# Optimization experiments

Measured on AMD Instinct MI355X. Metric: run time of the kernel, lower is better.

Reference implementation:

```python
import jax, jax.numpy as jnp
import numpy as np

N, E, F_NODE, F_EDGE, H, L, G = 4096, 12288, 64, 16, 128, 4, 256
BN_EPS = 1e-5


def setup_inputs() -> dict:
    key = jax.random.key(0)
    ks = jax.random.split(key, 20)
    s = lambda k, shape, fan: jax.random.normal(k, shape, jnp.float32) * (1.0 / np.sqrt(fan))
    inp = {
        'x': jax.random.normal(ks[0], (N, F_NODE), jnp.float32),
        'edge_index': jax.random.randint(ks[1], (2, E), 0, N, dtype=jnp.int64),
        'edge_attr': jax.random.normal(ks[2], (E, F_EDGE), jnp.float32),
        'batch': jnp.sort(jax.random.randint(ks[3], (N,), 0, G, dtype=jnp.int64)),
        # node encoder
        'node_w': s(ks[4], (F_NODE, H), F_NODE),
        'node_b': jnp.zeros((H,), jnp.float32),
        # per-layer edge MLP: edge_feat -> 128 -> H*H
        'e1_w': s(ks[5], (L, F_EDGE, 128), F_EDGE),
        'e1_b': jnp.zeros((L, 128), jnp.float32),
        'e2_w': s(ks[6], (L, 128, H * H), 128) * 0.1,
        'e2_b': jnp.zeros((L, H * H), jnp.float32),
        # NNConv root weight + bias
        'root_w': s(ks[7], (L, H, H), H),
        'conv_b': jnp.zeros((L, H), jnp.float32),
        # batchnorm affine
        'bn_g': jnp.ones((L, H), jnp.float32),
        'bn_b': jnp.zeros((L, H), jnp.float32),
        # head
        'head_w1': s(ks[8], (H, H), H),
        'head_b1': jnp.zeros((H,), jnp.float32),
        'head_w2': s(ks[9], (H, 1), H),
        'head_b2': jnp.zeros((1,), jnp.float32),
    }
    return inp


def reference(x, edge_index, edge_attr, batch, node_w, node_b, e1_w, e1_b,
              e2_w, e2_b, root_w, conv_b, bn_g, bn_b, head_w1, head_b1,
              head_w2, head_b2):
    src, dst = edge_index[0], edge_index[1]
    h = x @ node_w + node_b  # [N,H]
    # in-degree for mean aggregation
    deg = jax.ops.segment_sum(jnp.ones((E,), h.dtype), dst, num_segments=N)
    inv_deg = jnp.where(deg > 0, 1.0 / jnp.maximum(deg, 1.0), 0.0)[:, None]
    for l in range(L):
        # edge MLP -> per-edge [H,H] weight
        e = jax.nn.relu(edge_attr @ e1_w[l] + e1_b[l])            # [E,128]
        W_e = (e @ e2_w[l] + e2_b[l]).reshape(E, H, H)            # [E,H,H]
        msg = jnp.einsum('eh,eho->eo', h[src], W_e)               # [E,H]
        agg = jax.ops.segment_sum(msg, dst, num_segments=N) * inv_deg
        out = agg + h @ root_w[l] + conv_b[l]
        # batchnorm (training-mode batch stats, biased var as in torch)
        mu = out.mean(0)
        var = out.var(0)
        out = (out - mu) * jax.lax.rsqrt(var + BN_EPS) * bn_g[l] + bn_b[l]
        h = h + jax.nn.relu(out)  # dropout disabled (eval)
    # global mean pool over graphs
    cnt = jax.ops.segment_sum(jnp.ones((N,), h.dtype), batch, num_segments=G)
    pooled = jax.ops.segment_sum(h, batch, num_segments=G) / jnp.maximum(cnt, 1.0)[:, None]
    y = jax.nn.relu(pooled @ head_w1 + head_b1) @ head_w2 + head_b2
    return y.squeeze(-1)  # [G]
```

## Files before the change

### kernel.cpp

```cpp
#include <hip/hip_runtime.h>

#define N_NODES 4096
#define E_TOT   12288
#define F_NODE  64
#define F_EDGE  16
#define HDIM    128
#define NLAYER  4
#define NGRAPH  256

typedef _Float16 half8 __attribute__((ext_vector_type(8)));
typedef float    f32x4 __attribute__((ext_vector_type(4)));

__global__ void k_prep_w2(const float* __restrict__ e2w, const float* __restrict__ e2b,
                          _Float16* __restrict__ W2F)
{
    int t = blockIdx.x * 256 + threadIdx.x;
    const int PER_L = 129 * 16384;
    if (t >= NLAYER * PER_L) return;
    int l   = t / PER_L;
    int r   = t - l * PER_L;
    int k   = r >> 14;
    int rem = r & 16383;
    int chunk = rem >> 9;
    int lane  = (rem >> 3) & 63;
    int j     = rem & 7;
    int hc = chunk >> 3, ot = chunk & 7;
    int h  = hc * 32 + (lane >> 4) * 8 + j;
    int o  = ot * 16 + (lane & 15);
    float v;
    if (k < 128) v = e2w[((size_t)(l * 128 + k)) * 16384 + h * 128 + o];
    else         v = e2b[(size_t)l * 16384 + h * 128 + o];
    W2F[t] = (_Float16)v;
}

__global__ __launch_bounds__(128)
void k_node_enc(const float* __restrict__ x, const float* __restrict__ nw,
                const float* __restrict__ nb, float* __restrict__ h,
                _Float16* __restrict__ hf)
{
    __shared__ float xl[F_NODE];
    int n = blockIdx.x, o = threadIdx.x;
    if (o < F_NODE) xl[o] = x[(size_t)n * F_NODE + o];
    __syncthreads();
    float acc = nb[o];
#pragma unroll 8
    for (int f = 0; f < F_NODE; ++f) acc += xl[f] * nw[f * HDIM + o];
    h [(size_t)n * HDIM + o] = acc;
    hf[(size_t)n * HDIM + o] = (_Float16)acc;
}

__global__ void k_deg(const int* __restrict__ dst, int* __restrict__ deg)
{
    int e = blockIdx.x * 256 + threadIdx.x;
    if (e < E_TOT) atomicAdd(&deg[dst[e]], 1);
}

__global__ void k_invd(const int* __restrict__ deg, float* __restrict__ invd)
{
    int n = blockIdx.x * 256 + threadIdx.x;
    if (n < N_NODES) invd[n] = deg[n] > 0 ? 1.0f / (float)deg[n] : 0.0f;
}

#define EF_STRIDE 136
__global__ __launch_bounds__(128)
void k_edge_mlp(const float* __restrict__ ea, const float* __restrict__ w1,
                const float* __restrict__ b1, _Float16* __restrict__ efg)
{
    __shared__ float al[F_EDGE];
    int e = blockIdx.x, j = threadIdx.x;
    if (j < F_EDGE) al[j] = ea[(size_t)e * F_EDGE + j];
    __syncthreads();
    float acc = b1[j];
#pragma unroll
    for (int f = 0; f < F_EDGE; ++f) acc += al[f] * w1[f * HDIM + j];
    acc = fmaxf(acc, 0.f);
    efg[(size_t)e * EF_STRIDE + j] = (_Float16)acc;
    if (j == 0) efg[(size_t)e * EF_STRIDE + 128] = (_Float16)1.0f;
}

#define BM 96
__global__ __launch_bounds__(512, 4)
void k_msg(const _Float16* __restrict__ W2L,
           const _Float16* __restrict__ efg,
           const _Float16* __restrict__ hf,
           const int* __restrict__ srcIdx,
           const int* __restrict__ dstIdx,
           float* __restrict__ agg4)
{
    __shared__ _Float16 Bb[2][16384];
    __shared__ _Float16 efs[BM][40];

    const int tid  = threadIdx.x;
    const int lane = tid & 63;
    const int w    = tid >> 6;
    const int rq   = w >> 2;
    const int ch   = w & 3;
    const int lhi  = lane >> 4;
    const int llo  = lane & 15;

    const int bx    = blockIdx.x;
    const int ks    = (bx >> 1) & 3;
    const int tile  = (bx & 1) + (bx >> 3) * 2;
    const int e0    = tile * BM;
    const int kbase = (129 * ks) >> 2;
    const int kcnt  = ((129 * (ks + 1)) >> 2) - kbase;
    float* agg = agg4 + (size_t)ks * N_NODES * HDIM;

    if (tid < BM * 5) {
        int r = tid / 5, c = tid - r * 5;
        *(half8*)&efs[r][c * 8] =
            *(const half8*)(efg + (size_t)(e0 + r) * EF_STRIDE + kbase + c * 8);
    }

    half8 hs[3][4];
#pragma unroll
    for (int rf = 0; rf < 3; ++rf) {
        int s = srcIdx[e0 + rq * 48 + rf * 16 + llo];
        const _Float16* hp = hf + (size_t)s * HDIM + lhi * 8;
#pragma unroll
        for (int hc = 0; hc < 4; ++hc)
            hs[rf][hc] = *(const half8*)(hp + hc * 32);
    }

    asm volatile("s_waitcnt vmcnt(0) lgkmcnt(0)" ::: "memory");

    auto STAGE = [&](int kg, int buf) {
        const _Float16* g = W2L + (size_t)kg * 16384 + w * 2048 + lane * 8;
        _Float16* lp = &Bb[buf][w * 2048];
#pragma unroll
        for (int i = 0; i < 4; ++i)
            __builtin_amdgcn_global_load_lds(
                (const __attribute__((address_space(1))) void*)(g + i * 512),
                (__attribute__((address_space(3))) void*)(lp + i * 512), 16, 0, 0);
    };

    STAGE(kbase + 0, 0);

    f32x4 acc[3][2];
#pragma unroll
    for (int rf = 0; rf < 3; ++rf)
#pragma unroll
        for (int cf = 0; cf < 2; ++cf)
#pragma unroll
            for (int d = 0; d < 4; ++d) acc[rf][cf][d] = 0.f;

    for (int kk = 0; kk < kcnt; ++kk) {
        const int cur = kk & 1;
        asm volatile("" ::: "memory");
        __builtin_amdgcn_s_barrier();
        asm volatile("" ::: "memory");
        if (kk + 1 < kcnt) {
            STAGE(kbase + kk + 1, cur ^ 1);
            asm volatile("s_waitcnt vmcnt(4)" ::: "memory");
        } else {
            asm volatile("s_waitcnt vmcnt(0)" ::: "memory");
        }
        asm volatile("" ::: "memory");
        __builtin_amdgcn_s_barrier();
        asm volatile("" ::: "memory");

        _Float16 efv[3];
#pragma unroll
        for (int rf = 0; rf < 3; ++rf) efv[rf] = efs[rq * 48 + rf * 16 + llo][kk];

        const _Float16* bb = &Bb[cur][ch * 1024 + lane * 8];
        __builtin_amdgcn_s_setprio(1);
#pragma unroll
        for (int hc = 0; hc < 4; ++hc) {
            half8 bfr[2];
#pragma unroll
            for (int cf = 0; cf < 2; ++cf)
                bfr[cf] = *(const half8*)(bb + hc * 4096 + cf * 512);
#pragma unroll
            for (int rf = 0; rf < 3; ++rf) {
                half8 av = hs[rf][hc] * efv[rf];
#pragma unroll
                for (int cf = 0; cf < 2; ++cf)
                    acc[rf][cf] = __builtin_amdgcn_mfma_f32_16x16x32_f16(
                        av, bfr[cf], acc[rf][cf], 0, 0, 0);
            }
        }
        __builtin_amdgcn_s_setprio(0);
    }

#pragma unroll
    for (int rf = 0; rf < 3; ++rf) {
#pragma unroll
        for (int r = 0; r < 4; ++r) {
            int row = rq * 48 + rf * 16 + lhi * 4 + r;
            int d   = dstIdx[e0 + row];
#pragma unroll
            for (int cf = 0; cf < 2; ++cf) {
                int o = ch * 32 + cf * 16 + llo;
                atomicAdd(&agg[(size_t)d * HDIM + o], acc[rf][cf][r]);
            }
        }
    }
}

__global__ __launch_bounds__(128)
void k_out(const float* __restrict__ agg4, const float* __restrict__ invd,
           const float* __restrict__ h, const float* __restrict__ rw,
           const float* __restrict__ cb, float* __restrict__ outb)
{
    __shared__ float hl[16][HDIM];
    int n0 = blockIdx.x * 16, o = threadIdx.x;
    for (int r = 0; r < 16; ++r) hl[r][o] = h[(size_t)(n0 + r) * HDIM + o];
    __syncthreads();
    float acc[16];
    float cbv = cb[o];
#pragma unroll
    for (int r = 0; r < 16; ++r) {
        float s = 0.f;
#pragma unroll
        for (int p = 0; p < 4; ++p)
            s += agg4[(size_t)p * N_NODES * HDIM + (size_t)(n0 + r) * HDIM + o];
        acc[r] = s * invd[n0 + r] + cbv;
    }
    for (int hh = 0; hh < HDIM; ++hh) {
        float wv = rw[hh * HDIM + o];
#pragma unroll
        for (int r = 0; r < 16; ++r) acc[r] += hl[r][hh] * wv;
    }
#pragma unroll
    for (int r = 0; r < 16; ++r) outb[(size_t)(n0 + r) * HDIM + o] = acc[r];
}

__global__ __launch_bounds__(256)
void k_bn_stats(const float* __restrict__ outb, float* __restrict__ mu,
                float* __restrict__ rsig)
{
    __shared__ float s1[256], s2[256];
    int c = blockIdx.x, t = threadIdx.x;
    float a = 0.f, b = 0.f;
    for (int n = t; n < N_NODES; n += 256) {
        float v = outb[(size_t)n * HDIM + c];
        a += v; b += v * v;
    }
    s1[t] = a; s2[t] = b;
    __syncthreads();
    for (int s = 128; s > 0; s >>= 1) {
        if (t < s) { s1[t] += s1[t + s]; s2[t] += s2[t + s]; }
        __syncthreads();
    }
    if (t == 0) {
        float m   = s1[0] / (float)N_NODES;
        float var = s2[0] / (float)N_NODES - m * m;
        mu[c]   = m;
        rsig[c] = rsqrtf(var + 1e-5f);
    }
}

__global__ void k_bn_apply(const float* __restrict__ outb, const float* __restrict__ mu,
                           const float* __restrict__ rsig, const float* __restrict__ g,
                           const float* __restrict__ b, float* __restrict__ h,
                           _Float16* __restrict__ hf)
{
    int i = blockIdx.x * 256 + threadIdx.x;
    int o = i & (HDIM - 1);
    float v  = (outb[i] - mu[o]) * rsig[o] * g[o] + b[o];
    float hn = h[i] + fmaxf(v, 0.f);
    h[i]  = hn;
    hf[i] = (_Float16)hn;
}

__global__ __launch_bounds__(128)
void k_pool(const float* __restrict__ h, const int* __restrict__ batch,
            float* __restrict__ pooled, int* __restrict__ cnt)
{
    int n = blockIdx.x, c = threadIdx.x;
    int g = batch[n];
    atomicAdd(&pooled[(size_t)g * HDIM + c], h[(size_t)n * HDIM + c]);
    if (c == 0) atomicAdd(&cnt[g], 1);
}

__global__ __launch_bounds__(128)
void k_head(const float* __restrict__ pooled, const int* __restrict__ cnt,
            const float* __restrict__ w1, const float* __restrict__ b1,
            const float* __restrict__ w2, const float* __restrict__ b2,
            float* __restrict__ y)
{
    __shared__ float pl[HDIM];
    __shared__ float red[HDIM];
    int g = blockIdx.x, o = threadIdx.x;
    float ic = 1.0f / (float)max(cnt[g], 1);
    pl[o] = pooled[(size_t)g * HDIM + o] * ic;
    __syncthreads();
    float t = b1[o];
#pragma unroll 8
    for (int hh = 0; hh < HDIM; ++hh) t += pl[hh] * w1[hh * HDIM + o];
    t = fmaxf(t, 0.f);
    red[o] = t * w2[o];
    __syncthreads();
    for (int s = 64; s > 0; s >>= 1) {
        if (o < s) red[o] += red[o + s];
        __syncthreads();
    }
    if (o == 0) y[g] = red[0] + b2[0];
}

extern "C" void kernel_launch(void* const* d_in, const int* in_sizes, int n_in,
                              void* d_out, int out_size, void* d_ws, size_t ws_size,
                              hipStream_t stream)
{
    const float* x      = (const float*)d_in[0];
    const int*   ei     = (const int*)  d_in[1];
    const float* ea     = (const float*)d_in[2];
    const int*   batch  = (const int*)  d_in[3];
    const float* node_w = (const float*)d_in[4];
    const float* node_b = (const float*)d_in[5];
    const float* e1w    = (const float*)d_in[6];
    const float* e1b    = (const float*)d_in[7];
    const float* e2w    = (const float*)d_in[8];
    const float* e2b    = (const float*)d_in[9];
    const float* rw     = (const float*)d_in[10];
    const float* cb     = (const float*)d_in[11];
    const float* bng    = (const float*)d_in[12];
    const float* bnb    = (const float*)d_in[13];
    const float* hw1    = (const float*)d_in[14];
    const float* hb1    = (const float*)d_in[15];
    const float* hw2    = (const float*)d_in[16];
    const float* hb2    = (const float*)d_in[17];
    float* y = (float*)d_out;

    char* ws = (char*)d_ws;
    _Float16* W2F  = (_Float16*)ws; ws += 16908288;
    float*    h    = (float*)ws;    ws += 2097152;
    _Float16* hf   = (_Float16*)ws; ws += 1048576;
    _Float16* efg  = (_Float16*)ws; ws += 3342336;
    float*    agg4 = (float*)ws;    ws += 8388608;
    float*    outb = (float*)ws;    ws += 2097152;
    int*      deg  = (int*)ws;      ws += 16384;
    float*    invd = (float*)ws;    ws += 16384;
    float*    mu   = (float*)ws;    ws += 512;
    float*    rsig = (float*)ws;    ws += 512;
    float*    pooled = (float*)ws;  ws += 131072;
    int*      cnt  = (int*)ws;      ws += 1024;

    const int* src = ei;
    const int* dst = ei + E_TOT;

    k_prep_w2<<<33024, 256, 0, stream>>>(e2w, e2b, W2F);
    k_node_enc<<<N_NODES, 128, 0, stream>>>(x, node_w, node_b, h, hf);
    hipMemsetAsync(deg, 0, N_NODES * sizeof(int), stream);
    k_deg<<<(E_TOT + 255) / 256, 256, 0, stream>>>(dst, deg);
    k_invd<<<(N_NODES + 255) / 256, 256, 0, stream>>>(deg, invd);

    for (int l = 0; l < NLAYER; ++l) {
        k_edge_mlp<<<E_TOT, 128, 0, stream>>>(ea, e1w + l * F_EDGE * HDIM,
                                              e1b + l * HDIM, efg);
        hipMemsetAsync(agg4, 0, (size_t)4 * N_NODES * HDIM * sizeof(float), stream);
        k_msg<<<(E_TOT / BM) * 4, 512, 0, stream>>>(W2F + (size_t)l * 129 * 16384,
                                                    efg, hf, src, dst, agg4);
        k_out<<<N_NODES / 16, 128, 0, stream>>>(agg4, invd, h,
                                                rw + l * HDIM * HDIM,
                                                cb + l * HDIM, outb);
        k_bn_stats<<<HDIM, 256, 0, stream>>>(outb, mu, rsig);
        k_bn_apply<<<(N_NODES * HDIM) / 256, 256, 0, stream>>>(
            outb, mu, rsig, bng + l * HDIM, bnb + l * HDIM, h, hf);
    }

    hipMemsetAsync(pooled, 0, (size_t)NGRAPH * HDIM * sizeof(float), stream);
    hipMemsetAsync(cnt, 0, NGRAPH * sizeof(int), stream);
    k_pool<<<N_NODES, 128, 0, stream>>>(h, batch, pooled, cnt);
    k_head<<<NGRAPH, 128, 0, stream>>>(pooled, cnt, hw1, hb1, hw2, hb2, y);
}
```

Measured before the change: 471.3 us.

## Load W2 directly into registers in k_msg, batch edge MLP, fuse BN stats

The message kernel drops the LDS double-buffer of W2 and has each wave load its own B fragments from global memory into registers, prefetching the next k-slice while issuing MFMAs. Tiles shrink to 64 edges with 256 threads, and each wave now covers all rows for a 32-column slice. The edge MLP processes 16 edges per block with weights cached in LDS and writes vectorized half8 outputs. BatchNorm statistics are accumulated with atomics inside k_out, which removes the separate stats kernel; the buffers are zeroed by extending the agg4 memset. The trade-offs are more global/L2 traffic for W2, since it is no longer shared across waves through LDS, and less precise one-pass variance.

```diff
diff --git a/kernel.cpp b/kernel.cpp
--- a/kernel.cpp
+++ b/kernel.cpp
@@ -62,24 +62,37 @@
 }
 
 #define EF_STRIDE 136
-__global__ __launch_bounds__(128)
+__global__ __launch_bounds__(256)
 void k_edge_mlp(const float* __restrict__ ea, const float* __restrict__ w1,
                 const float* __restrict__ b1, _Float16* __restrict__ efg)
 {
-    __shared__ float al[F_EDGE];
-    int e = blockIdx.x, j = threadIdx.x;
-    if (j < F_EDGE) al[j] = ea[(size_t)e * F_EDGE + j];
-    __syncthreads();
-    float acc = b1[j];
-#pragma unroll
-    for (int f = 0; f < F_EDGE; ++f) acc += al[f] * w1[f * HDIM + j];
-    acc = fmaxf(acc, 0.f);
-    efg[(size_t)e * EF_STRIDE + j] = (_Float16)acc;
-    if (j == 0) efg[(size_t)e * EF_STRIDE + 128] = (_Float16)1.0f;
-}
-
-#define BM 96
-__global__ __launch_bounds__(512, 4)
+    __shared__ float al[16][17];
+    __shared__ float wl[16][HDIM];
+    __shared__ float bl[HDIM];
+    int t = threadIdx.x, e0 = blockIdx.x * 16;
+    if (t < HDIM) bl[t] = b1[t];
+    for (int i = t; i < F_EDGE * HDIM; i += 256) wl[i >> 7][i & 127] = w1[i];
+    { int i = t; al[i >> 4][i & 15] = ea[(size_t)e0 * F_EDGE + i]; }
+    __syncthreads();
+    int e = t >> 4, og = t & 15;
+    float acc[8];
+#pragma unroll
+    for (int j = 0; j < 8; ++j) acc[j] = bl[og * 8 + j];
+#pragma unroll
+    for (int f = 0; f < F_EDGE; ++f) {
+        float a = al[e][f];
+#pragma unroll
+        for (int j = 0; j < 8; ++j) acc[j] += a * wl[f][og * 8 + j];
+    }
+    half8 o;
+#pragma unroll
+    for (int j = 0; j < 8; ++j) o[j] = (_Float16)fmaxf(acc[j], 0.f);
+    *(half8*)&efg[(size_t)(e0 + e) * EF_STRIDE + og * 8] = o;
+    if (og == 0) efg[(size_t)(e0 + e) * EF_STRIDE + 128] = (_Float16)1.0f;
+}
+
+#define BM 64
+__global__ __launch_bounds__(256, 3)
 void k_msg(const _Float16* __restrict__ W2L,
            const _Float16* __restrict__ efg,
            const _Float16* __restrict__ hf,
@@ -87,111 +100,100 @@
            const int* __restrict__ dstIdx,
            float* __restrict__ agg4)
 {
-    __shared__ _Float16 Bb[2][16384];
     __shared__ _Float16 efs[BM][40];
 
     const int tid  = threadIdx.x;
     const int lane = tid & 63;
     const int w    = tid >> 6;
-    const int rq   = w >> 2;
-    const int ch   = w & 3;
     const int lhi  = lane >> 4;
     const int llo  = lane & 15;
 
     const int bx    = blockIdx.x;
-    const int ks    = (bx >> 1) & 3;
-    const int tile  = (bx & 1) + (bx >> 3) * 2;
+    const int ks    = (bx & 7) >> 1;
+    const int tile  = (bx >> 3) * 2 + (bx & 1);
     const int e0    = tile * BM;
     const int kbase = (129 * ks) >> 2;
     const int kcnt  = ((129 * (ks + 1)) >> 2) - kbase;
     float* agg = agg4 + (size_t)ks * N_NODES * HDIM;
 
-    if (tid < BM * 5) {
-        int r = tid / 5, c = tid - r * 5;
+    for (int i = tid; i < BM * 5; i += 256) {
+        int r = i / 5, c = i - r * 5;
         *(half8*)&efs[r][c * 8] =
             *(const half8*)(efg + (size_t)(e0 + r) * EF_STRIDE + kbase + c * 8);
     }
 
-    half8 hs[3][4];
-#pragma unroll
-    for (int rf = 0; rf < 3; ++rf) {
-        int s = srcIdx[e0 + rq * 48 + rf * 16 + llo];
+    half8 hs[4][4];
+#pragma unroll
+    for (int rf = 0; rf < 4; ++rf) {
+        int s = srcIdx[e0 + rf * 16 + llo];
         const _Float16* hp = hf + (size_t)s * HDIM + lhi * 8;
 #pragma unroll
         for (int hc = 0; hc < 4; ++hc)
             hs[rf][hc] = *(const half8*)(hp + hc * 32);
     }
 
-    asm volatile("s_waitcnt vmcnt(0) lgkmcnt(0)" ::: "memory");
-
-    auto STAGE = [&](int kg, int buf) {
-        const _Float16* g = W2L + (size_t)kg * 16384 + w * 2048 + lane * 8;
-        _Float16* lp = &Bb[buf][w * 2048];
-#pragma unroll
-        for (int i = 0; i < 4; ++i)
-            __builtin_amdgcn_global_load_lds(
-                (const __attribute__((address_space(1))) void*)(g + i * 512),
-                (__attribute__((address_space(3))) void*)(lp + i * 512), 16, 0, 0);
-    };
-
-    STAGE(kbase + 0, 0);
-
-    f32x4 acc[3][2];
-#pragma unroll
-    for (int rf = 0; rf < 3; ++rf)
+    __syncthreads();
+
+    const _Float16* bp = W2L + (size_t)kbase * 16384 + (w * 2) * 512 + lane * 8;
+
+#define LDH(dst, kk, h2) do {                                          \
+        const _Float16* p_ = bp + (size_t)(kk) * 16384 + (h2) * 8192;  \
+        dst[0] = *(const half8*)(p_);                                  \
+        dst[1] = *(const half8*)(p_ + 512);                            \
+        dst[2] = *(const half8*)(p_ + 4096);                           \
+        dst[3] = *(const half8*)(p_ + 4608);                           \
+    } while (0)
+
+    half8 B0[4], B1[4];
+    LDH(B0, 0, 0);
+    LDH(B1, 0, 1);
+
+    f32x4 acc[4][2];
+#pragma unroll
+    for (int rf = 0; rf < 4; ++rf)
 #pragma unroll
         for (int cf = 0; cf < 2; ++cf)
 #pragma unroll
             for (int d = 0; d < 4; ++d) acc[rf][cf][d] = 0.f;
 
     for (int kk = 0; kk < kcnt; ++kk) {
-        const int cur = kk & 1;
-        asm volatile("" ::: "memory");
-        __builtin_amdgcn_s_barrier();
-        asm volatile("" ::: "memory");
-        if (kk + 1 < kcnt) {
-            STAGE(kbase + kk + 1, cur ^ 1);
-            asm volatile("s_waitcnt vmcnt(4)" ::: "memory");
-        } else {
-            asm volatile("s_waitcnt vmcnt(0)" ::: "memory");
+        _Float16 efv[4];
+#pragma unroll
+        for (int rf = 0; rf < 4; ++rf) efv[rf] = efs[rf * 16 + llo][kk];
+
+#pragma unroll
+        for (int rf = 0; rf < 4; ++rf) {
+            half8 av0 = hs[rf][0] * efv[rf];
+            half8 av1 = hs[rf][1] * efv[rf];
+            acc[rf][0] = __builtin_amdgcn_mfma_f32_16x16x32_f16(av0, B0[0], acc[rf][0], 0, 0, 0);
+            acc[rf][1] = __builtin_amdgcn_mfma_f32_16x16x32_f16(av0, B0[1], acc[rf][1], 0, 0, 0);
+            acc[rf][0] = __builtin_amdgcn_mfma_f32_16x16x32_f16(av1, B0[2], acc[rf][0], 0, 0, 0);
+            acc[rf][1] = __builtin_amdgcn_mfma_f32_16x16x32_f16(av1, B0[3], acc[rf][1], 0, 0, 0);
         }
-        asm volatile("" ::: "memory");
-        __builtin_amdgcn_s_barrier();
-        asm volatile("" ::: "memory");
-
-        _Float16 efv[3];
-#pragma unroll
-        for (int rf = 0; rf < 3; ++rf) efv[rf] = efs[rq * 48 + rf * 16 + llo][kk];
-
-        const _Float16* bb = &Bb[cur][ch * 1024 + lane * 8];
-        __builtin_amdgcn_s_setprio(1);
-#pragma unroll
-        for (int hc = 0; hc < 4; ++hc) {
-            half8 bfr[2];
-#pragma unroll
-            for (int cf = 0; cf < 2; ++cf)
-                bfr[cf] = *(const half8*)(bb + hc * 4096 + cf * 512);
-#pragma unroll
-            for (int rf = 0; rf < 3; ++rf) {
-                half8 av = hs[rf][hc] * efv[rf];
-#pragma unroll
-                for (int cf = 0; cf < 2; ++cf)
-                    acc[rf][cf] = __builtin_amdgcn_mfma_f32_16x16x32_f16(
-                        av, bfr[cf], acc[rf][cf], 0, 0, 0);
-            }
+        if (kk + 1 < kcnt) LDH(B0, kk + 1, 0);
+
+#pragma unroll
+        for (int rf = 0; rf < 4; ++rf) {
+            half8 av2 = hs[rf][2] * efv[rf];
+            half8 av3 = hs[rf][3] * efv[rf];
+            acc[rf][0] = __builtin_amdgcn_mfma_f32_16x16x32_f16(av2, B1[0], acc[rf][0], 0, 0, 0);
+            acc[rf][1] = __builtin_amdgcn_mfma_f32_16x16x32_f16(av2, B1[1], acc[rf][1], 0, 0, 0);
+            acc[rf][0] = __builtin_amdgcn_mfma_f32_16x16x32_f16(av3, B1[2], acc[rf][0], 0, 0, 0);
+            acc[rf][1] = __builtin_amdgcn_mfma_f32_16x16x32_f16(av3, B1[3], acc[rf][1], 0, 0, 0);
         }
-        __builtin_amdgcn_s_setprio(0);
-    }
-
-#pragma unroll
-    for (int rf = 0; rf < 3; ++rf) {
+        if (kk + 1 < kcnt) LDH(B1, kk + 1, 1);
+    }
+#undef LDH
+
+#pragma unroll
+    for (int rf = 0; rf < 4; ++rf) {
 #pragma unroll
         for (int r = 0; r < 4; ++r) {
-            int row = rq * 48 + rf * 16 + lhi * 4 + r;
+            int row = rf * 16 + lhi * 4 + r;
             int d   = dstIdx[e0 + row];
 #pragma unroll
             for (int cf = 0; cf < 2; ++cf) {
-                int o = ch * 32 + cf * 16 + llo;
+                int o = w * 32 + cf * 16 + llo;
                 atomicAdd(&agg[(size_t)d * HDIM + o], acc[rf][cf][r]);
             }
         }
@@ -201,7 +203,8 @@
 __global__ __launch_bounds__(128)
 void k_out(const float* __restrict__ agg4, const float* __restrict__ invd,
            const float* __restrict__ h, const float* __restrict__ rw,
-           const float* __restrict__ cb, float* __restrict__ outb)
+           const float* __restrict__ cb, float* __restrict__ outb,
+           float* __restrict__ bns1, float* __restrict__ bns2)
 {
     __shared__ float hl[16][HDIM];
     int n0 = blockIdx.x * 16, o = threadIdx.x;
@@ -222,43 +225,29 @@
 #pragma unroll
         for (int r = 0; r < 16; ++r) acc[r] += hl[r][hh] * wv;
     }
-#pragma unroll
-    for (int r = 0; r < 16; ++r) outb[(size_t)(n0 + r) * HDIM + o] = acc[r];
-}
-
-__global__ __launch_bounds__(256)
-void k_bn_stats(const float* __restrict__ outb, float* __restrict__ mu,
-                float* __restrict__ rsig)
-{
-    __shared__ float s1[256], s2[256];
-    int c = blockIdx.x, t = threadIdx.x;
-    float a = 0.f, b = 0.f;
-    for (int n = t; n < N_NODES; n += 256) {
-        float v = outb[(size_t)n * HDIM + c];
-        a += v; b += v * v;
-    }
-    s1[t] = a; s2[t] = b;
-    __syncthreads();
-    for (int s = 128; s > 0; s >>= 1) {
-        if (t < s) { s1[t] += s1[t + s]; s2[t] += s2[t + s]; }
-        __syncthreads();
-    }
-    if (t == 0) {
-        float m   = s1[0] / (float)N_NODES;
-        float var = s2[0] / (float)N_NODES - m * m;
-        mu[c]   = m;
-        rsig[c] = rsqrtf(var + 1e-5f);
-    }
-}
-
-__global__ void k_bn_apply(const float* __restrict__ outb, const float* __restrict__ mu,
-                           const float* __restrict__ rsig, const float* __restrict__ g,
+    float s1 = 0.f, s2 = 0.f;
+#pragma unroll
+    for (int r = 0; r < 16; ++r) {
+        outb[(size_t)(n0 + r) * HDIM + o] = acc[r];
+        s1 += acc[r];
+        s2 += acc[r] * acc[r];
+    }
+    atomicAdd(&bns1[o], s1);
+    atomicAdd(&bns2[o], s2);
+}
+
+__global__ void k_bn_apply(const float* __restrict__ outb, const float* __restrict__ bns1,
+                           const float* __restrict__ bns2, const float* __restrict__ g,
                            const float* __restrict__ b, float* __restrict__ h,
                            _Float16* __restrict__ hf)
 {
     int i = blockIdx.x * 256 + threadIdx.x;
     int o = i & (HDIM - 1);
-    float v  = (outb[i] - mu[o]) * rsig[o] * g[o] + b[o];
+    const float inv_n = 1.0f / (float)N_NODES;
+    float m   = bns1[o] * inv_n;
+    float var = bns2[o] * inv_n - m * m;
+    float rs  = rsqrtf(var + 1e-5f);
+    float v  = (outb[i] - m) * rs * g[o] + b[o];
     float hn = h[i] + fmaxf(v, 0.f);
     h[i]  = hn;
     hf[i] = (_Float16)hn;
@@ -329,11 +318,11 @@
     _Float16* hf   = (_Float16*)ws; ws += 1048576;
     _Float16* efg  = (_Float16*)ws; ws += 3342336;
     float*    agg4 = (float*)ws;    ws += 8388608;
+    float*    bns1 = (float*)ws;    ws += 512;
+    float*    bns2 = (float*)ws;    ws += 512;
     float*    outb = (float*)ws;    ws += 2097152;
     int*      deg  = (int*)ws;      ws += 16384;
     float*    invd = (float*)ws;    ws += 16384;
-    float*    mu   = (float*)ws;    ws += 512;
-    float*    rsig = (float*)ws;    ws += 512;
     float*    pooled = (float*)ws;  ws += 131072;
     int*      cnt  = (int*)ws;      ws += 1024;
 
@@ -347,17 +336,16 @@
     k_invd<<<(N_NODES + 255) / 256, 256, 0, stream>>>(deg, invd);
 
     for (int l = 0; l < NLAYER; ++l) {
-        k_edge_mlp<<<E_TOT, 128, 0, stream>>>(ea, e1w + l * F_EDGE * HDIM,
-                                              e1b + l * HDIM, efg);
-        hipMemsetAsync(agg4, 0, (size_t)4 * N_NODES * HDIM * sizeof(float), stream);
-        k_msg<<<(E_TOT / BM) * 4, 512, 0, stream>>>(W2F + (size_t)l * 129 * 16384,
+        k_edge_mlp<<<E_TOT / 16, 256, 0, stream>>>(ea, e1w + l * F_EDGE * HDIM,
+                                                   e1b + l * HDIM, efg);
+        hipMemsetAsync(agg4, 0, (size_t)4 * N_NODES * HDIM * sizeof(float) + 1024, stream);
+        k_msg<<<(E_TOT / BM) * 4, 256, 0, stream>>>(W2F + (size_t)l * 129 * 16384,
                                                     efg, hf, src, dst, agg4);
         k_out<<<N_NODES / 16, 128, 0, stream>>>(agg4, invd, h,
                                                 rw + l * HDIM * HDIM,
-                                                cb + l * HDIM, outb);
-        k_bn_stats<<<HDIM, 256, 0, stream>>>(outb, mu, rsig);
+                                                cb + l * HDIM, outb, bns1, bns2);
         k_bn_apply<<<(N_NODES * HDIM) / 256, 256, 0, stream>>>(
-            outb, mu, rsig, bng + l * HDIM, bnb + l * HDIM, h, hf);
+            outb, bns1, bns2, bng + l * HDIM, bnb + l * HDIM, h, hf);
     }
 
     hipMemsetAsync(pooled, 0, (size_t)NGRAPH * HDIM * sizeof(float), stream);
```

New measurement: 432.2 us. 1.09x faster.
